# Kernel optimization log

Hardware: AMD Instinct MI355X
Metric: run time of the kernel (lower is better)

Reference implementation:

```python
import jax, jax.numpy as jnp
import numpy as np

N_NODES = 100000
N_EDGES = 1000000
C_IN, C_HID, C_OUT = 128, 64, 32


def _gcn_layer(x, W, b, src, dst, n):
    """PyG GCNConv with default add_self_loops=True, symmetric normalization.

    x: [N, in], W: [in, out], b: [out], src/dst: [E] int
    """
    h = x @ W  # [N, out] -- transform before aggregation
    # degree of each node counting the added self loop
    deg = jax.ops.segment_sum(jnp.ones_like(dst, dtype=h.dtype), dst, num_segments=n) + 1.0
    dinv = jax.lax.rsqrt(deg)  # deg >= 1 so always finite
    norm = dinv[src] * dinv[dst]  # [E]
    msg = h[src] * norm[:, None]  # [E, out]
    agg = jax.ops.segment_sum(msg, dst, num_segments=n)  # [N, out]
    # self-loop contribution: norm_ii = dinv_i * dinv_i
    out = agg + h * (dinv * dinv)[:, None]
    return out + b


def setup_inputs() -> dict:
    key = jax.random.key(0)
    k1, k2, k3, k4 = jax.random.split(key, 4)
    x = jax.random.normal(k1, (N_NODES, C_IN), dtype=jnp.float32)
    edge_index = jax.random.randint(k2, (2, N_EDGES), 0, N_NODES, dtype=jnp.int64)
    # Glorot-style init for the two GCN layers
    W1 = jax.random.normal(k3, (C_IN, C_HID), dtype=jnp.float32) / np.sqrt(C_IN)
    b1 = jnp.zeros((C_HID,), dtype=jnp.float32)
    W2 = jax.random.normal(k4, (C_HID, C_OUT), dtype=jnp.float32) / np.sqrt(C_HID)
    b2 = jnp.zeros((C_OUT,), dtype=jnp.float32)
    return {"x": x, "edge_index": edge_index, "W1": W1, "b1": b1, "W2": W2, "b2": b2}


def reference(x, edge_index, W1, b1, W2, b2):
    src, dst = edge_index[0], edge_index[1]
    n = x.shape[0]
    h = _gcn_layer(x, W1, b1, src, dst, n)
    h = jax.nn.relu(h)  # Dropout(0.1) is identity in eval mode
    out = _gcn_layer(h, W2, b2, src, dst, n)
    return out
```

## Files before the change

kernel.cpp:

```cpp
#include <hip/hip_runtime.h>
#include <hip/hip_fp16.h>

#define N_NODES 100000
#define N_EDGES 1000000
#define C_IN 128
#define C_HID 64
#define C_OUT 32
#define NB1 ((N_NODES + 255) / 256)
#define GT_BLOCKS ((N_NODES + 63) / 64)

__global__ __launch_bounds__(64) void k_detect(const unsigned int* __restrict__ ei,
                                               int* __restrict__ flag) {
    if (threadIdx.x == 0 && blockIdx.x == 0) {
        int is64 = 1;
        for (int i = 0; i < 64; ++i)
            if (ei[2 * i + 1] != 0u) { is64 = 0; break; }
        *flag = is64;
    }
}

__global__ __launch_bounds__(256) void k_rank(const unsigned int* __restrict__ ei,
                                              const int* __restrict__ flag,
                                              int* __restrict__ deg,
                                              int* __restrict__ rank) {
    const int T = gridDim.x * 256;
    const int t = blockIdx.x * 256 + threadIdx.x;
    const bool is64 = (*flag != 0);
    int d[4];
#pragma unroll
    for (int i = 0; i < 4; ++i) {
        int e = t + i * T;
        if (e < N_EDGES)
            d[i] = is64 ? ((const int2*)ei)[(size_t)N_EDGES + e].x
                        : (int)ei[(size_t)N_EDGES + e];
    }
    int r[4];
#pragma unroll
    for (int i = 0; i < 4; ++i) {
        int e = t + i * T;
        if (e < N_EDGES) r[i] = atomicAdd(&deg[d[i]], 1);
    }
#pragma unroll
    for (int i = 0; i < 4; ++i) {
        int e = t + i * T;
        if (e < N_EDGES) __builtin_nontemporal_store(r[i], &rank[e]);
    }
}

__global__ __launch_bounds__(256) void k_scan1(const int* __restrict__ deg,
                                               int* __restrict__ rowstart,
                                               int* __restrict__ blksum,
                                               float* __restrict__ dinv) {
    __shared__ int sm[256];
    int i = blockIdx.x * 256 + threadIdx.x;
    int v = (i < N_NODES) ? deg[i] : 0;
    if (i < N_NODES) dinv[i] = rsqrtf((float)v + 1.0f);
    sm[threadIdx.x] = v;
    __syncthreads();
    for (int o = 1; o < 256; o <<= 1) {
        int t = (threadIdx.x >= o) ? sm[threadIdx.x - o] : 0;
        __syncthreads();
        sm[threadIdx.x] += t;
        __syncthreads();
    }
    if (i < N_NODES) rowstart[i] = sm[threadIdx.x] - v;
    if (threadIdx.x == 255) blksum[blockIdx.x] = sm[255];
}

__global__ __launch_bounds__(512) void k_scan2(const int* __restrict__ blksum,
                                               int* __restrict__ blkoff) {
    __shared__ int sm[512];
    int v = (threadIdx.x < NB1) ? blksum[threadIdx.x] : 0;
    sm[threadIdx.x] = v;
    __syncthreads();
    for (int o = 1; o < 512; o <<= 1) {
        int t = (threadIdx.x >= o) ? sm[threadIdx.x - o] : 0;
        __syncthreads();
        sm[threadIdx.x] += t;
        __syncthreads();
    }
    if (threadIdx.x < NB1) blkoff[threadIdx.x] = sm[threadIdx.x] - v;
}

__global__ __launch_bounds__(256) void k_scan3(int* __restrict__ rowstart,
                                               const int* __restrict__ blkoff) {
    int i = blockIdx.x * 256 + threadIdx.x;
    if (i < N_NODES) rowstart[i] += blkoff[i >> 8];
    if (i == 0) rowstart[N_NODES] = N_EDGES;
}

__global__ __launch_bounds__(256) void k_fill2(const unsigned int* __restrict__ ei,
                                               const int* __restrict__ flag,
                                               const int* __restrict__ rowstart,
                                               const int* __restrict__ rank,
                                               int* __restrict__ esrc) {
    const int T = gridDim.x * 256;
    const int t = blockIdx.x * 256 + threadIdx.x;
    const bool is64 = (*flag != 0);
#pragma unroll
    for (int i = 0; i < 4; ++i) {
        int e = t + i * T;
        if (e < N_EDGES) {
            int s, d;
            if (is64) {
                s = ((const int2*)ei)[e].x;
                d = ((const int2*)ei)[(size_t)N_EDGES + e].x;
            } else {
                s = (int)ei[e];
                d = (int)ei[(size_t)N_EDGES + e];
            }
            int p = rowstart[d] + rank[e];
            __builtin_nontemporal_store(s, &esrc[p]);
        }
    }
}

__global__ __launch_bounds__(256) void k_gemm1(const float* __restrict__ x,
                                               const float* __restrict__ W1,
                                               const float* __restrict__ dinv,
                                               __half* __restrict__ hs1h) {
    __shared__ float w[C_IN * C_HID];
    __shared__ float xt[64 * C_IN];
    const int t = threadIdx.x;
    {
        const float4* W4 = (const float4*)W1;
        const float4* x4g = (const float4*)x;
        float4* w4 = (float4*)w;
        float4* xt4w = (float4*)xt;
        const size_t base = (size_t)blockIdx.x * 64 * (C_IN / 4);
        const size_t xmax = (size_t)N_NODES * (C_IN / 4) - 1;
#pragma unroll
        for (int j = 0; j < 8; ++j) {
            size_t idx = base + t + j * 256;
            if (idx > xmax) idx = xmax;
            xt4w[t + j * 256] = x4g[idx];
            w4[t + j * 256] = W4[t + j * 256];
        }
    }
    __syncthreads();
    const int c2 = t & 31;
    const int h  = (t >> 5) & 1;
    const int wid = t >> 6;
    const int lrow0 = wid * 16 + h * 8;
    const int grow0 = blockIdx.x * 64 + lrow0;
    const float4* xt4 = (const float4*)xt;

    float acc0[8] = {0, 0, 0, 0, 0, 0, 0, 0};
    float acc1[8] = {0, 0, 0, 0, 0, 0, 0, 0};
#pragma unroll 2
    for (int k4 = 0; k4 < C_IN / 4; ++k4) {
        float4 xv[8];
#pragma unroll
        for (int r = 0; r < 8; ++r)
            xv[r] = xt4[(lrow0 + r) * (C_IN / 4) + k4];
        float2 wv[4];
#pragma unroll
        for (int j = 0; j < 4; ++j)
            wv[j] = *reinterpret_cast<const float2*>(&w[(k4 * 4 + j) * C_HID + 2 * c2]);
#pragma unroll
        for (int r = 0; r < 8; ++r) {
            acc0[r] = fmaf(xv[r].x, wv[0].x, acc0[r]);
            acc1[r] = fmaf(xv[r].x, wv[0].y, acc1[r]);
            acc0[r] = fmaf(xv[r].y, wv[1].x, acc0[r]);
            acc1[r] = fmaf(xv[r].y, wv[1].y, acc1[r]);
            acc0[r] = fmaf(xv[r].z, wv[2].x, acc0[r]);
            acc1[r] = fmaf(xv[r].z, wv[2].y, acc1[r]);
            acc0[r] = fmaf(xv[r].w, wv[3].x, acc0[r]);
            acc1[r] = fmaf(xv[r].w, wv[3].y, acc1[r]);
        }
    }
    __half2* h2o = (__half2*)hs1h;
#pragma unroll
    for (int r = 0; r < 8; ++r) {
        int rr = grow0 + r;
        if (rr < N_NODES) {
            float dv = dinv[rr];
            h2o[(size_t)rr * 32 + c2] = __floats2half2_rn(acc0[r] * dv, acc1[r] * dv);
        }
    }
}

__global__ __launch_bounds__(256) void k_agg1(const int* __restrict__ rowstart,
                                              const int* __restrict__ esrc,
                                              const __half* __restrict__ hs1h,
                                              const float* __restrict__ dinv,
                                              const float* __restrict__ b1,
                                              float* __restrict__ y1) {
    const int node = blockIdx.x * 4 + (threadIdx.x >> 6);
    const int lane = threadIdx.x & 63;
    const int c2 = lane & 31;
    const int eo = lane >> 5;
    const __half2* h2 = (const __half2*)hs1h;
    const int beg = rowstart[node], end = rowstart[node + 1];
    float2 acc; acc.x = 0.f; acc.y = 0.f;
    int j = beg + eo;
    for (; j + 6 < end; j += 8) {
        int s0 = esrc[j], s1 = esrc[j + 2], s2 = esrc[j + 4], s3 = esrc[j + 6];
        float2 v0 = __half22float2(h2[(size_t)s0 * 32 + c2]);
        float2 v1 = __half22float2(h2[(size_t)s1 * 32 + c2]);
        float2 v2 = __half22float2(h2[(size_t)s2 * 32 + c2]);
        float2 v3 = __half22float2(h2[(size_t)s3 * 32 + c2]);
        acc.x += (v0.x + v1.x) + (v2.x + v3.x);
        acc.y += (v0.y + v1.y) + (v2.y + v3.y);
    }
    for (; j < end; j += 2) {
        float2 v = __half22float2(h2[(size_t)esrc[j] * 32 + c2]);
        acc.x += v.x; acc.y += v.y;
    }
    acc.x += __shfl_xor(acc.x, 32);
    acc.y += __shfl_xor(acc.y, 32);
    if (eo == 0) {
        float2 self = __half22float2(h2[(size_t)node * 32 + c2]);
        float dv = dinv[node];
        float2 o;
        o.x = fmaxf(fmaf(dv, acc.x + self.x, b1[2 * c2]), 0.f);
        o.y = fmaxf(fmaf(dv, acc.y + self.y, b1[2 * c2 + 1]), 0.f);
        reinterpret_cast<float2*>(y1)[(size_t)node * 32 + c2] = o;
    }
}

__global__ __launch_bounds__(256) void k_gemm2(const float* __restrict__ y1,
                                               const float* __restrict__ W2,
                                               const float* __restrict__ dinv,
                                               __half* __restrict__ hs2h) {
    __shared__ float w[C_HID * C_OUT];
    __shared__ float yt[64 * C_HID];
    const int t = threadIdx.x;
    {
        const float4* W4 = (const float4*)W2;
        const float4* y4g = (const float4*)y1;
        float4* w4 = (float4*)w;
        float4* yt4w = (float4*)yt;
        const size_t base = (size_t)blockIdx.x * 64 * (C_HID / 4);
        const size_t ymax = (size_t)N_NODES * (C_HID / 4) - 1;
#pragma unroll
        for (int j = 0; j < 4; ++j) {
            size_t idx = base + t + j * 256;
            if (idx > ymax) idx = ymax;
            yt4w[t + j * 256] = y4g[idx];
        }
#pragma unroll
        for (int j = 0; j < 2; ++j)
            w4[t + j * 256] = W4[t + j * 256];
    }
    __syncthreads();
    const int c2 = t & 15;
    const int rg = (t >> 4) & 3;
    const int wid = t >> 6;
    const int lrow0 = wid * 16 + rg * 4;
    const int grow0 = blockIdx.x * 64 + lrow0;
    const float4* yt4 = (const float4*)yt;

    float2 acc[4];
#pragma unroll
    for (int r = 0; r < 4; ++r) { acc[r].x = 0.f; acc[r].y = 0.f; }
#pragma unroll 2
    for (int k4 = 0; k4 < C_HID / 4; ++k4) {
        float4 yv[4];
#pragma unroll
        for (int r = 0; r < 4; ++r)
            yv[r] = yt4[(lrow0 + r) * (C_HID / 4) + k4];
        float2 wv[4];
#pragma unroll
        for (int j = 0; j < 4; ++j)
            wv[j] = *reinterpret_cast<const float2*>(&w[(k4 * 4 + j) * C_OUT + 2 * c2]);
#pragma unroll
        for (int r = 0; r < 4; ++r) {
            acc[r].x = fmaf(yv[r].x, wv[0].x, acc[r].x);
            acc[r].y = fmaf(yv[r].x, wv[0].y, acc[r].y);
            acc[r].x = fmaf(yv[r].y, wv[1].x, acc[r].x);
            acc[r].y = fmaf(yv[r].y, wv[1].y, acc[r].y);
            acc[r].x = fmaf(yv[r].z, wv[2].x, acc[r].x);
            acc[r].y = fmaf(yv[r].z, wv[2].y, acc[r].y);
            acc[r].x = fmaf(yv[r].w, wv[3].x, acc[r].x);
            acc[r].y = fmaf(yv[r].w, wv[3].y, acc[r].y);
        }
    }
    __half2* h2o = (__half2*)hs2h;
#pragma unroll
    for (int r = 0; r < 4; ++r) {
        int rr = grow0 + r;
        if (rr < N_NODES) {
            float dv = dinv[rr];
            h2o[(size_t)rr * 16 + c2] = __floats2half2_rn(acc[r].x * dv, acc[r].y * dv);
        }
    }
}

__global__ __launch_bounds__(256) void k_agg2(const int* __restrict__ rowstart,
                                              const int* __restrict__ esrc,
                                              const __half* __restrict__ hs2h,
                                              const float* __restrict__ dinv,
                                              const float* __restrict__ b2,
                                              float* __restrict__ out) {
    const int node = blockIdx.x * 4 + (threadIdx.x >> 6);
    const int lane = threadIdx.x & 63;
    const int c2 = lane & 15;
    const int eo = lane >> 4;
    const __half2* h2 = (const __half2*)hs2h;
    const int beg = rowstart[node], end = rowstart[node + 1];
    float2 acc; acc.x = 0.f; acc.y = 0.f;
    int j = beg + eo;
    for (; j + 12 < end; j += 16) {
        int s0 = esrc[j], s1 = esrc[j + 4], s2 = esrc[j + 8], s3 = esrc[j + 12];
        float2 v0 = __half22float2(h2[(size_t)s0 * 16 + c2]);
        float2 v1 = __half22float2(h2[(size_t)s1 * 16 + c2]);
        float2 v2 = __half22float2(h2[(size_t)s2 * 16 + c2]);
        float2 v3 = __half22float2(h2[(size_t)s3 * 16 + c2]);
        acc.x += (v0.x + v1.x) + (v2.x + v3.x);
        acc.y += (v0.y + v1.y) + (v2.y + v3.y);
    }
    for (; j < end; j += 4) {
        float2 v = __half22float2(h2[(size_t)esrc[j] * 16 + c2]);
        acc.x += v.x; acc.y += v.y;
    }
    acc.x += __shfl_xor(acc.x, 16);
    acc.y += __shfl_xor(acc.y, 16);
    acc.x += __shfl_xor(acc.x, 32);
    acc.y += __shfl_xor(acc.y, 32);
    if (eo == 0) {
        float2 self = __half22float2(h2[(size_t)node * 16 + c2]);
        float dv = dinv[node];
        float2 o;
        o.x = fmaf(dv, acc.x + self.x, b2[2 * c2]);
        o.y = fmaf(dv, acc.y + self.y, b2[2 * c2 + 1]);
        reinterpret_cast<float2*>(out)[(size_t)node * 16 + c2] = o;
    }
}

extern "C" void kernel_launch(void* const* d_in, const int* in_sizes, int n_in,
                              void* d_out, int out_size, void* d_ws, size_t ws_size,
                              hipStream_t stream) {
    const float* x  = (const float*)d_in[0];
    const unsigned int* ei = (const unsigned int*)d_in[1];
    const float* W1 = (const float*)d_in[2];
    const float* b1 = (const float*)d_in[3];
    const float* W2 = (const float*)d_in[4];
    const float* b2 = (const float*)d_in[5];
    float* out = (float*)d_out;

    char* ws = (char*)d_ws;
    size_t off = 0;
    auto take = [&](size_t bytes) {
        char* p = ws + off;
        off += (bytes + 255) & ~(size_t)255;
        return p;
    };
    int*    flag     = (int*)   take(256);
    int*    esrc     = (int*)   take((size_t)N_EDGES * 4);
    int*    rank     = (int*)   take((size_t)N_EDGES * 4);
    int*    deg      = (int*)   take((size_t)N_NODES * 4);
    int*    rowstart = (int*)   take((size_t)(N_NODES + 1) * 4);
    int*    blksum   = (int*)   take((size_t)NB1 * 4);
    int*    blkoff   = (int*)   take((size_t)NB1 * 4);
    float*  dinv     = (float*) take((size_t)N_NODES * 4);
    __half* hs1h     = (__half*)take((size_t)N_NODES * C_HID * 2);
    float*  y1       = (float*) take((size_t)N_NODES * C_HID * 4);
    __half* hs2h     = (__half*)take((size_t)N_NODES * C_OUT * 2);

    k_detect<<<1, 64, 0, stream>>>(ei, flag);
    hipMemsetAsync(deg, 0, (size_t)N_NODES * 4, stream);
    k_rank<<<1024, 256, 0, stream>>>(ei, flag, deg, rank);

    k_scan1<<<NB1, 256, 0, stream>>>(deg, rowstart, blksum, dinv);
    k_scan2<<<1, 512, 0, stream>>>(blksum, blkoff);
    k_scan3<<<NB1, 256, 0, stream>>>(rowstart, blkoff);

    k_fill2<<<1024, 256, 0, stream>>>(ei, flag, rowstart, rank, esrc);

    k_gemm1<<<GT_BLOCKS, 256, 0, stream>>>(x, W1, dinv, hs1h);
    k_agg1<<<N_NODES / 4, 256, 0, stream>>>(rowstart, esrc, hs1h, dinv, b1, y1);

    k_gemm2<<<GT_BLOCKS, 256, 0, stream>>>(y1, W2, dinv, hs2h);
    k_agg2<<<N_NODES / 4, 256, 0, stream>>>(rowstart, esrc, hs2h, dinv, b2, out);
}
```

Baseline: 310.7 us.

## Fuse layer-1 aggregation with layer-2 GEMM and batch gather loads

Merges the first aggregation and the second small GEMM into one persistent-wave kernel. Each wave aggregates a node row, applies bias and ReLU, stages the row in shared memory, and multiplies it by W2 held in registers. This drops the fp32 y1 intermediate buffer and one kernel launch. Both aggregation kernels now issue 8 or 4 predicated gathers per iteration for more memory-level parallelism, in exchange for higher register pressure and some wasted loads on low-degree nodes.

```diff
diff --git a/kernel.cpp b/kernel.cpp
--- a/kernel.cpp
+++ b/kernel.cpp
@@ -8,6 +8,7 @@
 #define C_OUT 32
 #define NB1 ((N_NODES + 255) / 256)
 #define GT_BLOCKS ((N_NODES + 63) / 64)
+#define AGG1_BLOCKS 6250
 
 __global__ __launch_bounds__(64) void k_detect(const unsigned int* __restrict__ ei,
                                                int* __restrict__ flag) {
@@ -180,110 +181,68 @@
     }
 }
 
-__global__ __launch_bounds__(256) void k_agg1(const int* __restrict__ rowstart,
-                                              const int* __restrict__ esrc,
-                                              const __half* __restrict__ hs1h,
-                                              const float* __restrict__ dinv,
-                                              const float* __restrict__ b1,
-                                              float* __restrict__ y1) {
-    const int node = blockIdx.x * 4 + (threadIdx.x >> 6);
+__global__ __launch_bounds__(256) void k_agg1g2(const int* __restrict__ rowstart,
+                                                const int* __restrict__ esrc,
+                                                const __half* __restrict__ hs1h,
+                                                const float* __restrict__ dinv,
+                                                const float* __restrict__ b1,
+                                                const float* __restrict__ W2,
+                                                __half* __restrict__ hs2h) {
+    __shared__ float2 yrow[4][32];
+    const int wid = threadIdx.x >> 6;
     const int lane = threadIdx.x & 63;
     const int c2 = lane & 31;
     const int eo = lane >> 5;
+    float Wreg[32];
+#pragma unroll
+    for (int kk = 0; kk < 16; ++kk) {
+        Wreg[2 * kk]     = W2[(32 * eo + 2 * kk) * C_OUT + c2];
+        Wreg[2 * kk + 1] = W2[(32 * eo + 2 * kk + 1) * C_OUT + c2];
+    }
     const __half2* h2 = (const __half2*)hs1h;
-    const int beg = rowstart[node], end = rowstart[node + 1];
-    float2 acc; acc.x = 0.f; acc.y = 0.f;
-    int j = beg + eo;
-    for (; j + 6 < end; j += 8) {
-        int s0 = esrc[j], s1 = esrc[j + 2], s2 = esrc[j + 4], s3 = esrc[j + 6];
-        float2 v0 = __half22float2(h2[(size_t)s0 * 32 + c2]);
-        float2 v1 = __half22float2(h2[(size_t)s1 * 32 + c2]);
-        float2 v2 = __half22float2(h2[(size_t)s2 * 32 + c2]);
-        float2 v3 = __half22float2(h2[(size_t)s3 * 32 + c2]);
-        acc.x += (v0.x + v1.x) + (v2.x + v3.x);
-        acc.y += (v0.y + v1.y) + (v2.y + v3.y);
-    }
-    for (; j < end; j += 2) {
-        float2 v = __half22float2(h2[(size_t)esrc[j] * 32 + c2]);
-        acc.x += v.x; acc.y += v.y;
-    }
-    acc.x += __shfl_xor(acc.x, 32);
-    acc.y += __shfl_xor(acc.y, 32);
-    if (eo == 0) {
+    const float2 bb = { b1[2 * c2], b1[2 * c2 + 1] };
+    const int waveId = blockIdx.x * 4 + wid;
+
+    for (int node = waveId; node < N_NODES; node += AGG1_BLOCKS * 4) {
+        const int beg = rowstart[node], end = rowstart[node + 1];
+        float2 acc; acc.x = 0.f; acc.y = 0.f;
+        for (int j0 = beg; j0 < end; j0 += 16) {
+            const int jj = j0 + eo;
+            int idx[8];
+#pragma unroll
+            for (int s = 0; s < 8; ++s) {
+                int j = jj + 2 * s;
+                idx[s] = esrc[j < end ? j : beg];
+            }
+            float2 v[8];
+#pragma unroll
+            for (int s = 0; s < 8; ++s)
+                v[s] = __half22float2(h2[(size_t)idx[s] * 32 + c2]);
+#pragma unroll
+            for (int s = 0; s < 8; ++s) {
+                if (jj + 2 * s < end) { acc.x += v[s].x; acc.y += v[s].y; }
+            }
+        }
+        acc.x += __shfl_xor(acc.x, 32);
+        acc.y += __shfl_xor(acc.y, 32);
+        const float dv = dinv[node];
         float2 self = __half22float2(h2[(size_t)node * 32 + c2]);
-        float dv = dinv[node];
-        float2 o;
-        o.x = fmaxf(fmaf(dv, acc.x + self.x, b1[2 * c2]), 0.f);
-        o.y = fmaxf(fmaf(dv, acc.y + self.y, b1[2 * c2 + 1]), 0.f);
-        reinterpret_cast<float2*>(y1)[(size_t)node * 32 + c2] = o;
-    }
-}
-
-__global__ __launch_bounds__(256) void k_gemm2(const float* __restrict__ y1,
-                                               const float* __restrict__ W2,
-                                               const float* __restrict__ dinv,
-                                               __half* __restrict__ hs2h) {
-    __shared__ float w[C_HID * C_OUT];
-    __shared__ float yt[64 * C_HID];
-    const int t = threadIdx.x;
-    {
-        const float4* W4 = (const float4*)W2;
-        const float4* y4g = (const float4*)y1;
-        float4* w4 = (float4*)w;
-        float4* yt4w = (float4*)yt;
-        const size_t base = (size_t)blockIdx.x * 64 * (C_HID / 4);
-        const size_t ymax = (size_t)N_NODES * (C_HID / 4) - 1;
-#pragma unroll
-        for (int j = 0; j < 4; ++j) {
-            size_t idx = base + t + j * 256;
-            if (idx > ymax) idx = ymax;
-            yt4w[t + j * 256] = y4g[idx];
-        }
-#pragma unroll
-        for (int j = 0; j < 2; ++j)
-            w4[t + j * 256] = W4[t + j * 256];
-    }
-    __syncthreads();
-    const int c2 = t & 15;
-    const int rg = (t >> 4) & 3;
-    const int wid = t >> 6;
-    const int lrow0 = wid * 16 + rg * 4;
-    const int grow0 = blockIdx.x * 64 + lrow0;
-    const float4* yt4 = (const float4*)yt;
-
-    float2 acc[4];
-#pragma unroll
-    for (int r = 0; r < 4; ++r) { acc[r].x = 0.f; acc[r].y = 0.f; }
-#pragma unroll 2
-    for (int k4 = 0; k4 < C_HID / 4; ++k4) {
-        float4 yv[4];
-#pragma unroll
-        for (int r = 0; r < 4; ++r)
-            yv[r] = yt4[(lrow0 + r) * (C_HID / 4) + k4];
-        float2 wv[4];
-#pragma unroll
-        for (int j = 0; j < 4; ++j)
-            wv[j] = *reinterpret_cast<const float2*>(&w[(k4 * 4 + j) * C_OUT + 2 * c2]);
-#pragma unroll
-        for (int r = 0; r < 4; ++r) {
-            acc[r].x = fmaf(yv[r].x, wv[0].x, acc[r].x);
-            acc[r].y = fmaf(yv[r].x, wv[0].y, acc[r].y);
-            acc[r].x = fmaf(yv[r].y, wv[1].x, acc[r].x);
-            acc[r].y = fmaf(yv[r].y, wv[1].y, acc[r].y);
-            acc[r].x = fmaf(yv[r].z, wv[2].x, acc[r].x);
-            acc[r].y = fmaf(yv[r].z, wv[2].y, acc[r].y);
-            acc[r].x = fmaf(yv[r].w, wv[3].x, acc[r].x);
-            acc[r].y = fmaf(yv[r].w, wv[3].y, acc[r].y);
-        }
-    }
-    __half2* h2o = (__half2*)hs2h;
-#pragma unroll
-    for (int r = 0; r < 4; ++r) {
-        int rr = grow0 + r;
-        if (rr < N_NODES) {
-            float dv = dinv[rr];
-            h2o[(size_t)rr * 16 + c2] = __floats2half2_rn(acc[r].x * dv, acc[r].y * dv);
-        }
+        float2 y;
+        y.x = fmaxf(fmaf(dv, acc.x + self.x, bb.x), 0.f);
+        y.y = fmaxf(fmaf(dv, acc.y + self.y, bb.y), 0.f);
+        yrow[wid][c2] = y;
+        __builtin_amdgcn_wave_barrier();
+        float o = 0.f;
+#pragma unroll
+        for (int kk = 0; kk < 16; ++kk) {
+            float2 yv = yrow[wid][16 * eo + kk];
+            o = fmaf(yv.x, Wreg[2 * kk], o);
+            o = fmaf(yv.y, Wreg[2 * kk + 1], o);
+        }
+        __builtin_amdgcn_wave_barrier();
+        o += __shfl_xor(o, 32);
+        if (eo == 0)
+            hs2h[(size_t)node * C_OUT + c2] = __float2half(o * dv);
     }
 }
 
@@ -300,19 +259,22 @@
     const __half2* h2 = (const __half2*)hs2h;
     const int beg = rowstart[node], end = rowstart[node + 1];
     float2 acc; acc.x = 0.f; acc.y = 0.f;
-    int j = beg + eo;
-    for (; j + 12 < end; j += 16) {
-        int s0 = esrc[j], s1 = esrc[j + 4], s2 = esrc[j + 8], s3 = esrc[j + 12];
-        float2 v0 = __half22float2(h2[(size_t)s0 * 16 + c2]);
-        float2 v1 = __half22float2(h2[(size_t)s1 * 16 + c2]);
-        float2 v2 = __half22float2(h2[(size_t)s2 * 16 + c2]);
-        float2 v3 = __half22float2(h2[(size_t)s3 * 16 + c2]);
-        acc.x += (v0.x + v1.x) + (v2.x + v3.x);
-        acc.y += (v0.y + v1.y) + (v2.y + v3.y);
-    }
-    for (; j < end; j += 4) {
-        float2 v = __half22float2(h2[(size_t)esrc[j] * 16 + c2]);
-        acc.x += v.x; acc.y += v.y;
+    for (int j0 = beg; j0 < end; j0 += 16) {
+        const int jj = j0 + eo;
+        int idx[4];
+#pragma unroll
+        for (int s = 0; s < 4; ++s) {
+            int j = jj + 4 * s;
+            idx[s] = esrc[j < end ? j : beg];
+        }
+        float2 v[4];
+#pragma unroll
+        for (int s = 0; s < 4; ++s)
+            v[s] = __half22float2(h2[(size_t)idx[s] * 16 + c2]);
+#pragma unroll
+        for (int s = 0; s < 4; ++s) {
+            if (jj + 4 * s < end) { acc.x += v[s].x; acc.y += v[s].y; }
+        }
     }
     acc.x += __shfl_xor(acc.x, 16);
     acc.y += __shfl_xor(acc.y, 16);
@@ -355,7 +317,6 @@
     int*    blkoff   = (int*)   take((size_t)NB1 * 4);
     float*  dinv     = (float*) take((size_t)N_NODES * 4);
     __half* hs1h     = (__half*)take((size_t)N_NODES * C_HID * 2);
-    float*  y1       = (float*) take((size_t)N_NODES * C_HID * 4);
     __half* hs2h     = (__half*)take((size_t)N_NODES * C_OUT * 2);
 
     k_detect<<<1, 64, 0, stream>>>(ei, flag);
@@ -369,8 +330,8 @@
     k_fill2<<<1024, 256, 0, stream>>>(ei, flag, rowstart, rank, esrc);
 
     k_gemm1<<<GT_BLOCKS, 256, 0, stream>>>(x, W1, dinv, hs1h);
-    k_agg1<<<N_NODES / 4, 256, 0, stream>>>(rowstart, esrc, hs1h, dinv, b1, y1);
-
-    k_gemm2<<<GT_BLOCKS, 256, 0, stream>>>(y1, W2, dinv, hs2h);
+
+    k_agg1g2<<<AGG1_BLOCKS, 256, 0, stream>>>(rowstart, esrc, hs1h, dinv, b1, W2, hs2h);
+
     k_agg2<<<N_NODES / 4, 256, 0, stream>>>(rowstart, esrc, hs2h, dinv, b2, out);
 }
```

Measured after the change: 291.8 us. 6.1% less time.
